# Performance work log

Hardware: AMD Instinct MI355X
Metric: run time of the kernel (lower is better)

## Reference

```python
import jax, jax.numpy as jnp
import numpy as np
from jax import lax

EPS_RADIUS = 1e-3  # eps_radius from __init__


def setup_inputs() -> dict:
    key = jax.random.key(0)
    ks = jax.random.split(key, 8)
    Bsz, L, H, N, O = 16, 4096, 512, 512, 512
    n_pairs = N // 2
    return {
        "input": jax.random.normal(ks[0], (Bsz, L, H), dtype=jnp.float32),
        "state": jnp.zeros((Bsz, N), dtype=jnp.float32),
        "S": 0.1 * jax.random.normal(ks[1], (N, N), dtype=jnp.float32),
        "rho_raw": 0.01 * jax.random.normal(ks[2], (n_pairs,), dtype=jnp.float32),
        "theta": 0.01 * jax.random.normal(ks[3], (n_pairs,), dtype=jnp.float32),
        "K12_raw": 0.5 * jax.random.normal(ks[4], (N, H), dtype=jnp.float32),
        "K21_raw": 0.5 * jax.random.normal(ks[5], (O, N), dtype=jnp.float32),
        "K22_raw": 0.5 * jax.random.normal(ks[6], (O, H), dtype=jnp.float32),
        "log_gamma": jnp.zeros((), dtype=jnp.float32),  # gamma = 1.0
    }


def _dense_ssm_matrices(S, rho_raw, theta, K12_raw, K21_raw, K22_raw, log_gamma):
    N = S.shape[0]
    n_pairs = N // 2
    # K11 structured: block-diag 2x2 rotation-scaling blocks
    rho = jax.nn.sigmoid(rho_raw) * (1.0 - EPS_RADIUS)
    c, s = jnp.cos(theta), jnp.sin(theta)
    ii = jnp.arange(n_pairs) * 2
    K11 = jnp.zeros((N, N), dtype=S.dtype)
    K11 = (K11.at[ii, ii].set(rho * c)
               .at[ii, ii + 1].set(-rho * s)
               .at[ii + 1, ii].set(rho * s)
               .at[ii + 1, ii + 1].set(rho * c))
    # assemble full K and spectrally normalize (exact norm via SVD)
    K_raw = jnp.block([[K11, K12_raw], [K21_raw, K22_raw]])
    sigma = jnp.maximum(jnp.linalg.norm(K_raw, ord=2), 1e-5)
    K = K_raw / (sigma + 0.002)
    K11n = K[:N, :N]
    K12n = K[:N, N:]
    K21n = K[N:, :N]
    K22n = K[N:, N:]
    gamma = jnp.exp(log_gamma)
    Sinv = jnp.linalg.inv(S)
    A = Sinv @ K11n @ S          # (N, N)
    B = gamma * (Sinv @ K12n)    # (N, H)
    C = K21n @ S                 # (O, N)
    D = gamma * K22n             # (O, H)
    return A, B, C, D


def reference(input, state, S, rho_raw, theta, K12_raw, K21_raw, K22_raw, log_gamma):
    A, B, C, D = _dense_ssm_matrices(S, rho_raw, theta, K12_raw, K21_raw, K22_raw, log_gamma)
    u = input  # (Bsz, L, H)
    Bu = jnp.einsum('blh,nh->lbn', u, B)  # precompute input projections, (L, Bsz, N)

    def step(x, bu_t):
        x_new = x @ A.T + bu_t  # (Bsz, N)
        return x_new, x_new

    _, xs = lax.scan(step, state, Bu)  # xs: (L, Bsz, N), states x_1..x_L
    # y_t = C x_t + D u_t uses pre-states x_0..x_{L-1}
    pre = jnp.concatenate([state[None], xs[:-1]], axis=0)  # (L, Bsz, N)
    y = jnp.einsum('lbn,on->blo', pre, C) + jnp.einsum('blh,oh->blo', u, D)
    return y
```

## Files before the change

kernel.cpp:

```cpp
#include <hip/hip_runtime.h>
#include <stdint.h>


#define LM 40
#define CHUNK 128
#define WARM 12
#define LBLK 32

typedef float f32x4 __attribute__((ext_vector_type(4)));
typedef __bf16 bf16x8 __attribute__((ext_vector_type(8)));
typedef unsigned int u32;
typedef unsigned short u16;

static __device__ __forceinline__ u16 f2bf(float f){
  u32 u = __float_as_uint(f);
  u32 r = (u + 0x7fffu + ((u >> 16) & 1u)) >> 16;
  return (u16)r;
}

static __device__ __forceinline__ float kraw_at(int i, int j,
    const float* rho_raw, const float* theta,
    const float* K12, const float* K21, const float* K22){
  if (i < 512){
    if (j < 512){
      if ((i >> 1) != (j >> 1)) return 0.f;
      int p = i >> 1;
      float rho = (1.f / (1.f + expf(-rho_raw[p]))) * 0.999f;
      float c = cosf(theta[p]), s = sinf(theta[p]);
      return ((i & 1) == 0) ? (((j & 1) == 0) ? rho * c : -rho * s)
                            : (((j & 1) == 0) ? rho * s :  rho * c);
    }
    return K12[i * 512 + (j - 512)];
  }
  if (j < 512) return K21[(i - 512) * 512 + j];
  return K22[(i - 512) * 512 + (j - 512)];
}

__global__ __launch_bounds__(256) void build_KT(const float* rho_raw, const float* theta,
    const float* K12, const float* K21, const float* K22, u16* KTbf){
  int idx = blockIdx.x * 256 + threadIdx.x;
  int j = idx >> 10, i = idx & 1023;
  KTbf[idx] = f2bf(kraw_at(i, j, rho_raw, theta, K12, K21, K22));
}

__global__ __launch_bounds__(256) void init_scalars(double* alpha, double* nrm2, u32* flags){
  int t = threadIdx.x;
  if (t < 64) alpha[t] = 0.0;
  if (t < 64) nrm2[t] = 0.0;
  for (int i = t; i < 2048; i += 256) flags[i] = 0u;
}

__global__ __launch_bounds__(256, 1) void lanczos_G(const float* __restrict__ G,
    float* W0, float* W1, double* alphaOut, double* nrm2Out, u32* flags){
  __shared__ __align__(16) float vl[1024];
  __shared__ float red[8];
  int t = threadIdx.x, wave = t >> 6, lane = t & 63;
  int row0 = blockIdx.x * 32;
  float* wbuf[2] = {W0, W1};

  f32x4 greg[8][4];
  {
    const float* gbase = G + (size_t)(row0 + wave * 8) * 1024 + lane * 4;
    #pragma unroll
    for (int rr = 0; rr < 8; ++rr)
      #pragma unroll
      for (int i2 = 0; i2 < 4; ++i2)
        greg[rr][i2] = *(const f32x4*)(gbase + (size_t)rr * 1024 + i2 * 256);
  }

  float vprevreg[4] = {0.f, 0.f, 0.f, 0.f};
  float n2tot;
  {
    float s = 0.f;
    #pragma unroll
    for (int k = 0; k < 4; ++k){
      int i = t + 256 * k;
      float v = sinf(0.613f * (float)i + 0.271f) + 0.3f * sinf(0.0247f * (float)i + 1.3f);
      vl[i] = v;
      s += v * v;
    }
    #pragma unroll
    for (int off = 32; off; off >>= 1) s += __shfl_down(s, off);
    if (lane == 0) red[wave] = s;
    __syncthreads();
    n2tot = (red[0] + red[1]) + (red[2] + red[3]);
  }
  float scal = 1.f / sqrtf(n2tot);
  float betacoef = 0.f;

  for (int j = 1; j <= LM; ++j){
    float* Wt = wbuf[j & 1];
    {
      f32x4 vreg[4];
      #pragma unroll
      for (int i2 = 0; i2 < 4; ++i2)
        vreg[i2] = *((const f32x4*)vl + lane + 64 * i2);
      float yv[8];
      #pragma unroll
      for (int rr = 0; rr < 8; ++rr){
        float s = 0.f;
        #pragma unroll
        for (int i2 = 0; i2 < 4; ++i2){
          f32x4 g = greg[rr][i2], v = vreg[i2];
          s += g[0] * v[0] + g[1] * v[1] + g[2] * v[2] + g[3] * v[3];
        }
        #pragma unroll
        for (int off = 32; off; off >>= 1) s += __shfl_down(s, off);
        yv[rr] = s;
      }
      if (lane == 0){
        #pragma unroll
        for (int rr = 0; rr < 8; ++rr)
          __hip_atomic_store(&Wt[row0 + wave * 8 + rr], yv[rr],
                             __ATOMIC_RELAXED, __HIP_MEMORY_SCOPE_AGENT);
      }
    }

    asm volatile("s_waitcnt vmcnt(0)" ::: "memory");
    __syncthreads();
    if (t == 0)
      __hip_atomic_store(&flags[blockIdx.x * 16], (u32)j,
                         __ATOMIC_RELAXED, __HIP_MEMORY_SCOPE_AGENT);
    if (t < LBLK){
      while (__hip_atomic_load(&flags[t * 16],
                               __ATOMIC_RELAXED, __HIP_MEMORY_SCOPE_AGENT) < (u32)j)
        __builtin_amdgcn_s_sleep(1);
    }
    __syncthreads();

    float yr[4], vr[4];
    float dotp = 0.f;
    #pragma unroll
    for (int k = 0; k < 4; ++k){
      int i = t + 256 * k;
      yr[k] = __hip_atomic_load(&Wt[i], __ATOMIC_RELAXED, __HIP_MEMORY_SCOPE_AGENT);
      vr[k] = vl[i];
      dotp += vr[k] * yr[k];
    }
    #pragma unroll
    for (int off = 32; off; off >>= 1) dotp += __shfl_down(dotp, off);
    if (lane == 0) red[wave] = dotp;
    __syncthreads();
    float dot = (red[0] + red[1]) + (red[2] + red[3]);
    float alpha_f = dot * scal * scal;

    float n2 = 0.f;
    #pragma unroll
    for (int k = 0; k < 4; ++k){
      float vh = vr[k] * scal;
      float wv = yr[k] * scal - alpha_f * vh - betacoef * vprevreg[k];
      vprevreg[k] = vh;
      vl[t + 256 * k] = wv;
      n2 += wv * wv;
    }
    #pragma unroll
    for (int off = 32; off; off >>= 1) n2 += __shfl_down(n2, off);
    if (lane == 0) red[4 + wave] = n2;
    __syncthreads();
    n2tot = (red[4] + red[5]) + (red[6] + red[7]);
    if (n2tot < 1e-30f) n2tot = 1e-30f;

    if (blockIdx.x == 0 && t == 0){
      alphaOut[j] = (double)alpha_f;
      nrm2Out[j]  = (double)n2tot;
    }
    betacoef = sqrtf(n2tot);
    scal = 1.f / betacoef;
  }
}

__global__ __launch_bounds__(256) void finalize_sigma(const double* alpha, const double* beta2,
    const float* rho_raw, const float* theta, const float* log_gamma,
    float* scal, float2* coef){
  __shared__ double sa[LM], sb2[LM + 1];
  __shared__ float sh_inv;
  int t = threadIdx.x;
  if (t < LM) sa[t] = alpha[t];
  if (t < LM + 1) sb2[t] = beta2[t];
  __syncthreads();
  if (t < 64){
    int lane = t;
    double lo = sa[0], hi = sa[0], bmax = 0.0;
    for (int i = 0; i < LM; ++i){
      if (sa[i] > lo) lo = sa[i];
      double bl = (i > 0) ? sqrt(fmax(sb2[i], 0.0)) : 0.0;
      double br = (i < LM - 1) ? sqrt(fmax(sb2[i + 1], 0.0)) : 0.0;
      double g = sa[i] + bl + br;
      if (g > hi) hi = g;
      if (i < LM - 1 && sb2[i + 1] > bmax) bmax = sb2[i + 1];
    }
    hi = hi + 1e-6 * fabs(hi) + 1e-20;
    lo = lo - 1e-6 * fabs(lo) - 1e-20;
    double pivmin = 1e-30 * bmax + 1e-300;
    for (int round = 0; round < 6; ++round){
      double x = lo + (hi - lo) * ((double)(lane + 1) / 65.0);
      double d = sa[0] - x; int cnt = (d < 0.0);
      for (int i = 1; i < LM; ++i){
        if (fabs(d) < pivmin) d = -pivmin;
        d = (sa[i] - x) - sb2[i] / d;
        cnt += (d < 0.0);
      }
      unsigned long long mk = __ballot(cnt >= LM);
      int bpos = (mk == 0ULL) ? 64 : (__ffsll((unsigned long long)mk) - 1);
      double xlo = __shfl(x, (bpos == 0) ? 0 : bpos - 1);
      double xhi = __shfl(x, (bpos == 64) ? 63 : bpos);
      double nlo = (bpos == 0) ? lo : xlo;
      double nhi = (bpos == 64) ? hi : xhi;
      lo = nlo; hi = nhi;
    }
    if (lane == 0){
      double lam = 0.5 * (lo + hi);
      double sig = (lam > 0.0) ? sqrt(lam) : 0.0;
      if (sig < 1e-5) sig = 1e-5;
      double spp = sig + 0.002;
      float inv = (float)(1.0 / spp);
      float g = expf(log_gamma[0]);
      scal[0] = inv; scal[1] = g; scal[2] = g * inv;
      sh_inv = inv;
    }
  }
  __syncthreads();
  float inv = sh_inv;
  float rho = (1.f / (1.f + expf(-rho_raw[t]))) * 0.999f;
  float c = cosf(theta[t]), s = sinf(theta[t]);
  coef[t] = make_float2(rho * c * inv, rho * s * inv);
}

__global__ __launch_bounds__(256) void conv_u(const float4* u4, u16* X){
  long g = (long)blockIdx.x * 256 + threadIdx.x;
  float4 v = u4[g];
  int h4 = (int)(g & 127);
  long row = g >> 7;
  u16* dst = X + row * 1024 + 512 + h4 * 4;
  u32 lo = (u32)f2bf(v.x) | ((u32)f2bf(v.y) << 16);
  u32 hi = (u32)f2bf(v.z) | ((u32)f2bf(v.w) << 16);
  *((uint2*)dst) = make_uint2(lo, hi);
}

__global__ __launch_bounds__(256) void conv_w12(const float4* src, u16* dst){
  long g = (long)blockIdx.x * 256 + threadIdx.x;
  float4 v = src[g];
  u32 lo = (u32)f2bf(v.x) | ((u32)f2bf(v.y) << 16);
  u32 hi = (u32)f2bf(v.z) | ((u32)f2bf(v.w) << 16);
  ((uint2*)dst)[g] = make_uint2(lo, hi);
}

__global__ __launch_bounds__(256) void build_wcat(const float* K21, const float* K22,
    const float* scal, u16* W){
  int idx = blockIdx.x * 256 + threadIdx.x;
  int o = idx >> 10, c = idx & 1023;
  float inv = scal[0], gi = scal[2];
  float v = (c < 512) ? K21[o * 512 + c] * inv : K22[o * 512 + (c - 512)] * gi;
  W[idx] = f2bf(v);
}

__global__ __launch_bounds__(256) void w0_matvec(const float* S, const float* state, float* w0){
  int idx = blockIdx.x * 256 + threadIdx.x;
  int b = idx >> 9, n = idx & 511;
  const float* sr = S + n * 512;
  const float* st = state + b * 512;
  float acc = 0.f;
  for (int m2 = 0; m2 < 512; ++m2) acc += sr[m2] * st[m2];
  w0[idx] = acc;
}

__global__ __launch_bounds__(256) void scan_kernel(const u32* Bu, const float2* coef,
    const float* w0, const float* scal, u16* X){
  int b = blockIdx.x >> 5;
  int c = blockIdx.x & 31;
  int p = threadIdx.x;
  float2 ab = coef[p];
  float gi = scal[2];
  int t0 = c * CHUNK;
  float wx, wy; int t;
  if (c == 0){ wx = w0[b * 512 + 2 * p]; wy = w0[b * 512 + 2 * p + 1]; t = 0; }
  else { wx = 0.f; wy = 0.f; t = t0 - WARM; }
  const u32* bub = Bu + (size_t)b * 4096 * 256;
  u16* xb = X + (size_t)b * 4096 * 1024;
  for (; t < t0; ++t){
    u32 v = bub[(size_t)t * 256 + p];
    float bx = __uint_as_float(v << 16);
    float by = __uint_as_float(v & 0xffff0000u);
    float nx = ab.x * wx - ab.y * wy + gi * bx;
    float ny = ab.y * wx + ab.x * wy + gi * by;
    wx = nx; wy = ny;
  }
  for (; t < t0 + CHUNK; ++t){
    u32 pk = (u32)f2bf(wx) | ((u32)f2bf(wy) << 16);
    *(u32*)(xb + (size_t)t * 1024 + 2 * p) = pk;
    u32 v = bub[(size_t)t * 256 + p];
    float bx = __uint_as_float(v << 16);
    float by = __uint_as_float(v & 0xffff0000u);
    float nx = ab.x * wx - ab.y * wy + gi * bx;
    float ny = ab.y * wx + ab.x * wy + gi * by;
    wx = nx; wy = ny;
  }
}

static __device__ __forceinline__ void gload16(const u16* g, u16* l){
  __builtin_amdgcn_global_load_lds((const __attribute__((address_space(1))) u32*)g,
                                   (__attribute__((address_space(3))) u32*)l, 16, 0, 0);
}

template <typename OT>
__global__ __launch_bounds__(256) void gemm_nt(const u16* __restrict__ A, int lda,
    const u16* __restrict__ B, int ldb, OT* __restrict__ C, int ldc, int K, int ntn){
  __shared__ u16 As[128 * 64];
  __shared__ u16 Bs[128 * 64];
  int g = blockIdx.x;
  int xcd = g & 7, local = g >> 3;
  int mper = gridDim.x >> 3; mper /= ntn;
  int bn = local % ntn;
  int bm = xcd * mper + local / ntn;
  int t = threadIdx.x, lane = t & 63, wave = t >> 6;
  int lrow = t >> 3;
  int swz = (((t & 7) ^ (lrow & 7)) << 3);
  const u16* Ag = A + (size_t)(bm * 128 + lrow) * lda + swz;
  const u16* Bg = B + (size_t)(bn * 128 + lrow) * ldb + swz;
  u16* Asd = As + t * 8;
  u16* Bsd = Bs + t * 8;
  f32x4 acc[4][4];
  #pragma unroll
  for (int mi = 0; mi < 4; ++mi)
    #pragma unroll
    for (int ni = 0; ni < 4; ++ni) acc[mi][ni] = (f32x4){0.f, 0.f, 0.f, 0.f};
  int wm = (wave & 1) << 6, wn = (wave >> 1) << 6;
  int fr = lane & 15, cbb = lane >> 4;
  for (int kt = 0; kt < K; kt += 64){
    __syncthreads();
    #pragma unroll
    for (int r = 0; r < 4; ++r){
      gload16(Ag + (size_t)(r * 32) * lda + kt, Asd + r * 2048);
      gload16(Bg + (size_t)(r * 32) * ldb + kt, Bsd + r * 2048);
    }
    __syncthreads();
    #pragma unroll
    for (int kk = 0; kk < 2; ++kk){
      bf16x8 af[4], bfr[4];
      #pragma unroll
      for (int mi = 0; mi < 4; ++mi){
        int row = wm + mi * 16 + fr;
        int pcb = ((kk << 2) + cbb) ^ (fr & 7);
        af[mi] = *(const bf16x8*)(As + row * 64 + pcb * 8);
      }
      #pragma unroll
      for (int ni = 0; ni < 4; ++ni){
        int row = wn + ni * 16 + fr;
        int pcb = ((kk << 2) + cbb) ^ (fr & 7);
        bfr[ni] = *(const bf16x8*)(Bs + row * 64 + pcb * 8);
      }
      #pragma unroll
      for (int mi = 0; mi < 4; ++mi)
        #pragma unroll
        for (int ni = 0; ni < 4; ++ni)
          acc[mi][ni] = __builtin_amdgcn_mfma_f32_16x16x32_bf16(af[mi], bfr[ni], acc[mi][ni], 0, 0, 0);
    }
  }
  int rq = lane >> 4;
  #pragma unroll
  for (int mi = 0; mi < 4; ++mi)
    #pragma unroll
    for (int ni = 0; ni < 4; ++ni){
      size_t base = (size_t)(bm * 128 + wm + mi * 16 + rq * 4) * ldc
                  + (size_t)(bn * 128 + wn + ni * 16 + fr);
      #pragma unroll
      for (int r = 0; r < 4; ++r){
        if constexpr (sizeof(OT) == 4) C[base + (size_t)r * ldc] = acc[mi][ni][r];
        else                           C[base + (size_t)r * ldc] = (OT)f2bf(acc[mi][ni][r]);
      }
    }
}

extern "C" void kernel_launch(void* const* d_in, const int* in_sizes, int n_in,
                              void* d_out, int out_size, void* d_ws, size_t ws_size,
                              hipStream_t stream){
  const float* u        = (const float*)d_in[0];
  const float* state    = (const float*)d_in[1];
  const float* S        = (const float*)d_in[2];
  const float* rho_raw  = (const float*)d_in[3];
  const float* theta    = (const float*)d_in[4];
  const float* K12      = (const float*)d_in[5];
  const float* K21      = (const float*)d_in[6];
  const float* K22      = (const float*)d_in[7];
  const float* log_gamma= (const float*)d_in[8];

  char* w = (char*)d_ws;
  size_t off = 0;
  auto alloc = [&](size_t bytes)->void*{
    void* p = w + off;
    off = (off + bytes + 255) & ~(size_t)255;
    return p;
  };
  double* alpha = (double*)alloc(64 * 8);
  double* nrm2  = (double*)alloc(64 * 8);
  u32*    flags = (u32*)alloc(2048 * 4);
  float*  scal  = (float*)alloc(64);
  float2* coef  = (float2*)alloc(256 * 8);
  float*  W0    = (float*)alloc(1024 * 4);
  float*  W1    = (float*)alloc(1024 * 4);
  float*  w0    = (float*)alloc(16 * 512 * 4);
  u16*    KTbf  = (u16*)alloc((size_t)1024 * 1024 * 2);
  float*  G     = (float*)alloc((size_t)1024 * 1024 * 4);
  u16*    W12   = (u16*)alloc((size_t)512 * 512 * 2);
  u16*    Wcat  = (u16*)alloc((size_t)512 * 1024 * 2);
  u16*    Xb    = (u16*)alloc((size_t)65536 * 1024 * 2);
  u16*    Bu    = (u16*)d_out;

  init_scalars<<<1, 256, 0, stream>>>(alpha, nrm2, flags);
  build_KT<<<4096, 256, 0, stream>>>(rho_raw, theta, K12, K21, K22, KTbf);
  gemm_nt<float><<<64, 256, 0, stream>>>(KTbf, 1024, KTbf, 1024, G, 1024, 1024, 8);
  lanczos_G<<<LBLK, 256, 0, stream>>>(G, W0, W1, alpha, nrm2, flags);
  finalize_sigma<<<1, 256, 0, stream>>>(alpha + 1, nrm2, rho_raw, theta, log_gamma, scal, coef);

  conv_u<<<32768, 256, 0, stream>>>((const float4*)u, Xb);
  conv_w12<<<256, 256, 0, stream>>>((const float4*)K12, W12);
  build_wcat<<<2048, 256, 0, stream>>>(K21, K22, scal, Wcat);
  w0_matvec<<<32, 256, 0, stream>>>(S, state, w0);

  gemm_nt<u16><<<2048, 256, 0, stream>>>(Xb + 512, 1024, W12, 512, Bu, 512, 512, 4);
  scan_kernel<<<512, 256, 0, stream>>>((const u32*)Bu, coef, w0, scal, Xb);
  gemm_nt<float><<<2048, 256, 0, stream>>>(Xb, 1024, Wcat, 1024, (float*)d_out, 512, 1024, 4);
}
```

Before: 657.8 us.

## Tag Lanczos results with iteration stamps and fuse small prep kernels

```diff
diff --git a/kernel.cpp b/kernel.cpp
--- a/kernel.cpp
+++ b/kernel.cpp
@@ -10,6 +10,7 @@
 typedef float f32x4 __attribute__((ext_vector_type(4)));
 typedef __bf16 bf16x8 __attribute__((ext_vector_type(8)));
 typedef unsigned int u32;
+typedef unsigned long long u64;
 typedef unsigned short u16;
 
 static __device__ __forceinline__ u16 f2bf(float f){
@@ -37,26 +38,25 @@
 }
 
 __global__ __launch_bounds__(256) void build_KT(const float* rho_raw, const float* theta,
-    const float* K12, const float* K21, const float* K22, u16* KTbf){
+    const float* K12, const float* K21, const float* K22, u16* KTbf,
+    double* alpha, double* nrm2, u64* rec){
+  if (blockIdx.x == 4096){
+    int t = threadIdx.x;
+    if (t < 64){ alpha[t] = 0.0; nrm2[t] = 0.0; }
+    for (int i = t; i < 2048; i += 256) rec[i] = 0ull;
+    return;
+  }
   int idx = blockIdx.x * 256 + threadIdx.x;
   int j = idx >> 10, i = idx & 1023;
   KTbf[idx] = f2bf(kraw_at(i, j, rho_raw, theta, K12, K21, K22));
 }
 
-__global__ __launch_bounds__(256) void init_scalars(double* alpha, double* nrm2, u32* flags){
-  int t = threadIdx.x;
-  if (t < 64) alpha[t] = 0.0;
-  if (t < 64) nrm2[t] = 0.0;
-  for (int i = t; i < 2048; i += 256) flags[i] = 0u;
-}
-
 __global__ __launch_bounds__(256, 1) void lanczos_G(const float* __restrict__ G,
-    float* W0, float* W1, double* alphaOut, double* nrm2Out, u32* flags){
+    u64* rec, double* alphaOut, double* nrm2Out){
   __shared__ __align__(16) float vl[1024];
   __shared__ float red[8];
   int t = threadIdx.x, wave = t >> 6, lane = t & 63;
   int row0 = blockIdx.x * 32;
-  float* wbuf[2] = {W0, W1};
 
   f32x4 greg[8][4];
   {
@@ -89,13 +89,13 @@
   float betacoef = 0.f;
 
   for (int j = 1; j <= LM; ++j){
-    float* Wt = wbuf[j & 1];
+    u64* rb = rec + ((j & 1) ? 0 : 1024);
     {
       f32x4 vreg[4];
       #pragma unroll
       for (int i2 = 0; i2 < 4; ++i2)
         vreg[i2] = *((const f32x4*)vl + lane + 64 * i2);
-      float yv[8];
+      u64 myrec = 0ull;
       #pragma unroll
       for (int rr = 0; rr < 8; ++rr){
         float s = 0.f;
@@ -105,38 +105,40 @@
           s += g[0] * v[0] + g[1] * v[1] + g[2] * v[2] + g[3] * v[3];
         }
         #pragma unroll
-        for (int off = 32; off; off >>= 1) s += __shfl_down(s, off);
-        yv[rr] = s;
-      }
-      if (lane == 0){
+        for (int off = 32; off; off >>= 1) s += __shfl_xor(s, off);
+        if (lane == rr)
+          myrec = ((u64)(u32)j << 32) | (u64)__float_as_uint(s);
+      }
+      if (lane < 8)
+        __hip_atomic_store(&rb[row0 + wave * 8 + lane], myrec,
+                           __ATOMIC_RELAXED, __HIP_MEMORY_SCOPE_AGENT);
+    }
+
+    float yr[4], vr[4];
+    {
+      u32 need = 0xFu;
+      u64 rv[4];
+      while (need){
         #pragma unroll
-        for (int rr = 0; rr < 8; ++rr)
-          __hip_atomic_store(&Wt[row0 + wave * 8 + rr], yv[rr],
-                             __ATOMIC_RELAXED, __HIP_MEMORY_SCOPE_AGENT);
-      }
-    }
-
-    asm volatile("s_waitcnt vmcnt(0)" ::: "memory");
-    __syncthreads();
-    if (t == 0)
-      __hip_atomic_store(&flags[blockIdx.x * 16], (u32)j,
-                         __ATOMIC_RELAXED, __HIP_MEMORY_SCOPE_AGENT);
-    if (t < LBLK){
-      while (__hip_atomic_load(&flags[t * 16],
-                               __ATOMIC_RELAXED, __HIP_MEMORY_SCOPE_AGENT) < (u32)j)
-        __builtin_amdgcn_s_sleep(1);
-    }
-    __syncthreads();
-
-    float yr[4], vr[4];
+        for (int k = 0; k < 4; ++k){
+          if (need & (1u << k)){
+            u64 r = __hip_atomic_load(&rb[t + 256 * k],
+                                      __ATOMIC_RELAXED, __HIP_MEMORY_SCOPE_AGENT);
+            if ((u32)(r >> 32) == (u32)j){ rv[k] = r; need &= ~(1u << k); }
+          }
+        }
+        if (need) __builtin_amdgcn_s_sleep(1);
+      }
+      #pragma unroll
+      for (int k = 0; k < 4; ++k){
+        yr[k] = __uint_as_float((u32)rv[k]);
+        vr[k] = vl[t + 256 * k];
+      }
+    }
+
     float dotp = 0.f;
     #pragma unroll
-    for (int k = 0; k < 4; ++k){
-      int i = t + 256 * k;
-      yr[k] = __hip_atomic_load(&Wt[i], __ATOMIC_RELAXED, __HIP_MEMORY_SCOPE_AGENT);
-      vr[k] = vl[i];
-      dotp += vr[k] * yr[k];
-    }
+    for (int k = 0; k < 4; ++k) dotp += vr[k] * yr[k];
     #pragma unroll
     for (int off = 32; off; off >>= 1) dotp += __shfl_down(dotp, off);
     if (lane == 0) red[wave] = dotp;
@@ -226,23 +228,33 @@
   coef[t] = make_float2(rho * c * inv, rho * s * inv);
 }
 
-__global__ __launch_bounds__(256) void conv_u(const float4* u4, u16* X){
-  long g = (long)blockIdx.x * 256 + threadIdx.x;
-  float4 v = u4[g];
-  int h4 = (int)(g & 127);
-  long row = g >> 7;
-  u16* dst = X + row * 1024 + 512 + h4 * 4;
-  u32 lo = (u32)f2bf(v.x) | ((u32)f2bf(v.y) << 16);
-  u32 hi = (u32)f2bf(v.z) | ((u32)f2bf(v.w) << 16);
-  *((uint2*)dst) = make_uint2(lo, hi);
-}
-
-__global__ __launch_bounds__(256) void conv_w12(const float4* src, u16* dst){
-  long g = (long)blockIdx.x * 256 + threadIdx.x;
-  float4 v = src[g];
-  u32 lo = (u32)f2bf(v.x) | ((u32)f2bf(v.y) << 16);
-  u32 hi = (u32)f2bf(v.z) | ((u32)f2bf(v.w) << 16);
-  ((uint2*)dst)[g] = make_uint2(lo, hi);
+__global__ __launch_bounds__(256) void prep_main(const float4* u4, u16* X,
+    const float4* k12_4, u16* W12, const float* S, const float* state, float* w0){
+  int blk = blockIdx.x;
+  if (blk < 32768){
+    long g = (long)blk * 256 + threadIdx.x;
+    float4 v = u4[g];
+    int h4 = (int)(g & 127);
+    long row = g >> 7;
+    u16* dst = X + row * 1024 + 512 + h4 * 4;
+    u32 lo = (u32)f2bf(v.x) | ((u32)f2bf(v.y) << 16);
+    u32 hi = (u32)f2bf(v.z) | ((u32)f2bf(v.w) << 16);
+    *((uint2*)dst) = make_uint2(lo, hi);
+  } else if (blk < 32768 + 256){
+    long g = (long)(blk - 32768) * 256 + threadIdx.x;
+    float4 v = k12_4[g];
+    u32 lo = (u32)f2bf(v.x) | ((u32)f2bf(v.y) << 16);
+    u32 hi = (u32)f2bf(v.z) | ((u32)f2bf(v.w) << 16);
+    ((uint2*)W12)[g] = make_uint2(lo, hi);
+  } else {
+    int idx = (blk - 33024) * 256 + threadIdx.x;
+    int b = idx >> 9, n = idx & 511;
+    const float* sr = S + n * 512;
+    const float* st = state + b * 512;
+    float acc = 0.f;
+    for (int m2 = 0; m2 < 512; ++m2) acc += sr[m2] * st[m2];
+    w0[idx] = acc;
+  }
 }
 
 __global__ __launch_bounds__(256) void build_wcat(const float* K21, const float* K22,
@@ -252,16 +264,6 @@
   float inv = scal[0], gi = scal[2];
   float v = (c < 512) ? K21[o * 512 + c] * inv : K22[o * 512 + (c - 512)] * gi;
   W[idx] = f2bf(v);
-}
-
-__global__ __launch_bounds__(256) void w0_matvec(const float* S, const float* state, float* w0){
-  int idx = blockIdx.x * 256 + threadIdx.x;
-  int b = idx >> 9, n = idx & 511;
-  const float* sr = S + n * 512;
-  const float* st = state + b * 512;
-  float acc = 0.f;
-  for (int m2 = 0; m2 < 512; ++m2) acc += sr[m2] * st[m2];
-  w0[idx] = acc;
 }
 
 __global__ __launch_bounds__(256) void scan_kernel(const u32* Bu, const float2* coef,
@@ -393,11 +395,9 @@
   };
   double* alpha = (double*)alloc(64 * 8);
   double* nrm2  = (double*)alloc(64 * 8);
-  u32*    flags = (u32*)alloc(2048 * 4);
+  u64*    rec   = (u64*)alloc(2048 * 8);
   float*  scal  = (float*)alloc(64);
   float2* coef  = (float2*)alloc(256 * 8);
-  float*  W0    = (float*)alloc(1024 * 4);
-  float*  W1    = (float*)alloc(1024 * 4);
   float*  w0    = (float*)alloc(16 * 512 * 4);
   u16*    KTbf  = (u16*)alloc((size_t)1024 * 1024 * 2);
   float*  G     = (float*)alloc((size_t)1024 * 1024 * 4);
@@ -406,16 +406,13 @@
   u16*    Xb    = (u16*)alloc((size_t)65536 * 1024 * 2);
   u16*    Bu    = (u16*)d_out;
 
-  init_scalars<<<1, 256, 0, stream>>>(alpha, nrm2, flags);
-  build_KT<<<4096, 256, 0, stream>>>(rho_raw, theta, K12, K21, K22, KTbf);
+  build_KT<<<4097, 256, 0, stream>>>(rho_raw, theta, K12, K21, K22, KTbf, alpha, nrm2, rec);
   gemm_nt<float><<<64, 256, 0, stream>>>(KTbf, 1024, KTbf, 1024, G, 1024, 1024, 8);
-  lanczos_G<<<LBLK, 256, 0, stream>>>(G, W0, W1, alpha, nrm2, flags);
+  lanczos_G<<<LBLK, 256, 0, stream>>>(G, rec, alpha, nrm2);
   finalize_sigma<<<1, 256, 0, stream>>>(alpha + 1, nrm2, rho_raw, theta, log_gamma, scal, coef);
 
-  conv_u<<<32768, 256, 0, stream>>>((const float4*)u, Xb);
-  conv_w12<<<256, 256, 0, stream>>>((const float4*)K12, W12);
+  prep_main<<<33056, 256, 0, stream>>>((const float4*)u, Xb, (const float4*)K12, W12, S, state, w0);
   build_wcat<<<2048, 256, 0, stream>>>(K21, K22, scal, Wcat);
-  w0_matvec<<<32, 256, 0, stream>>>(S, state, w0);
 
   gemm_nt<u16><<<2048, 256, 0, stream>>>(Xb + 512, 1024, W12, 512, Bu, 512, 512, 4);
   scan_kernel<<<512, 256, 0, stream>>>((const u32*)Bu, coef, w0, scal, Xb);
```

Measured after the change: 618.2 us. 1.06x faster.
